# Optimization experiments

Hardware: AMD Instinct MI355X
Metric: run time of the kernel (lower is better)

Reference implementation:

```python
import jax, jax.numpy as jnp
import numpy as np

D_MODEL = 16   # output feature dim of channel_proj
D_STATE = 8
D_CONV = 2
D_INNER = 4    # expand * inner mamba d_model (2*2)
DT_RANK = 1    # ceil(2/16)
NUM_PAIRS = 36
B, W, T = 8, 8, 1024


def setup_inputs() -> dict:
    key = jax.random.key(0)
    ks = jax.random.split(key, 12)
    s = 0.5
    return {
        "raw_signals": jax.random.normal(ks[0], (B, W, NUM_PAIRS, 2, T), jnp.float32),
        "in_proj_w": jax.random.normal(ks[1], (2 * D_INNER, 2), jnp.float32) * s,
        "conv_w": jax.random.normal(ks[2], (D_INNER, D_CONV), jnp.float32) * s,
        "conv_b": jax.random.normal(ks[3], (D_INNER,), jnp.float32) * 0.1,
        "x_proj_w": jax.random.normal(ks[4], (DT_RANK + 2 * D_STATE, D_INNER), jnp.float32) * s,
        "dt_proj_w": jax.random.normal(ks[5], (D_INNER, DT_RANK), jnp.float32) * s,
        "dt_proj_b": jax.random.normal(ks[6], (D_INNER,), jnp.float32) * 0.1,
        # S4D-real init: A_log = log(arange(1..d_state)) per inner channel
        "A_log": jnp.log(jnp.broadcast_to(jnp.arange(1, D_STATE + 1, dtype=jnp.float32), (D_INNER, D_STATE))),
        "D_skip": jnp.ones((D_INNER,), jnp.float32),
        "out_proj_w": jax.random.normal(ks[7], (2, D_INNER), jnp.float32) * s,
        "proj_w": jax.random.normal(ks[8], (D_MODEL, 2), jnp.float32) * s,
        "proj_b": jax.random.normal(ks[9], (D_MODEL,), jnp.float32) * 0.1,
    }


def _mamba_forward(x_in, in_proj_w, conv_w, conv_b, x_proj_w, dt_proj_w,
                   dt_proj_b, A_log, D_skip, out_proj_w):
    # x_in: (N, T, 2)
    N, Tlen, _ = x_in.shape
    xz = jnp.einsum('ntc,dc->ntd', x_in, in_proj_w)          # (N,T,2*d_inner)
    x, z = jnp.split(xz, 2, axis=-1)                          # (N,T,d_inner) each
    # causal depthwise conv1d, kernel size D_CONV
    xp = jnp.pad(x, ((0, 0), (D_CONV - 1, 0), (0, 0)))
    x = sum(xp[:, k:k + Tlen] * conv_w[:, k] for k in range(D_CONV)) + conv_b
    x = jax.nn.silu(x)
    # input-dependent dt, B, C
    x_dbl = jnp.einsum('ntd,ed->nte', x, x_proj_w)            # (N,T,dt_rank+2*d_state)
    dt, Bm, Cm = jnp.split(x_dbl, [DT_RANK, DT_RANK + D_STATE], axis=-1)
    dt = jax.nn.softplus(jnp.einsum('ntr,dr->ntd', dt, dt_proj_w) + dt_proj_b)
    A = -jnp.exp(A_log)                                       # (d_inner,d_state)
    deltaA = jnp.exp(dt[..., None] * A)                       # (N,T,d_inner,d_state)
    deltaBx = dt[..., None] * Bm[:, :, None, :] * x[..., None]

    def step(h, inputs):
        dA_t, dBx_t, c_t = inputs
        h = dA_t * h + dBx_t                                  # (N,d_inner,d_state)
        y_t = jnp.einsum('nds,ns->nd', h, c_t)
        return h, y_t

    h0 = jnp.zeros((N, D_INNER, D_STATE), x.dtype)
    _, ys = jax.lax.scan(
        step, h0,
        (deltaA.transpose(1, 0, 2, 3), deltaBx.transpose(1, 0, 2, 3), Cm.transpose(1, 0, 2)))
    y = ys.transpose(1, 0, 2) + x * D_skip                    # (N,T,d_inner)
    y = y * jax.nn.silu(z)
    return jnp.einsum('ntd,cd->ntc', y, out_proj_w)           # (N,T,2)


def reference(raw_signals, in_proj_w, conv_w, conv_b, x_proj_w, dt_proj_w,
              dt_proj_b, A_log, D_skip, out_proj_w, proj_w, proj_b):
    Bsz, Wn, P, C, Tlen = raw_signals.shape
    # per-window loop in torch does identical math -> flatten windows into batch
    x_in = raw_signals.transpose(0, 1, 2, 4, 3).reshape(-1, Tlen, C)  # (B*W*P, T, 2)
    out = _mamba_forward(x_in, in_proj_w, conv_w, conv_b, x_proj_w, dt_proj_w,
                         dt_proj_b, A_log, D_skip, out_proj_w)
    feat = out.mean(axis=1)                                   # (B*W*P, 2)
    proj = jax.nn.relu(feat @ proj_w.T + proj_b)              # dropout is eval no-op
    proj = proj.reshape(Bsz, Wn, P, -1)                       # (B,W,P,d_model)
    return proj.mean(axis=2)                                  # (B,W,d_model)
```

## Files before the change

### kernel.cpp

```cpp
#include <hip/hip_runtime.h>
#include <hip/hip_fp16.h>


typedef float v2f __attribute__((ext_vector_type(2)));

#define TT 1024
#define TC 32
#define NSEGS 8
#define SEGLEN (TT / NSEGS)
#define NCHUNK (SEGLEN / TC)
#define NUM_PAIRS 36
#define NSEQ 2304

#define DTDS_ROW 34
#define BC_OFF 272
#define BC_STRIDE 36
#define PER_HALF_STRIDE 560
#define PER_WAVE (2 * PER_HALF_STRIDE)
#define STAGE_TOTAL (4 * PER_WAVE)

__device__ __forceinline__ float fast_silu(float v) {
    float e = __builtin_amdgcn_exp2f(v * -1.4426950408889634f);
    return v * __builtin_amdgcn_rcpf(1.0f + e);
}
__device__ __forceinline__ float fast_softplus(float v) {
    float e = __builtin_amdgcn_exp2f(v * 1.4426950408889634f);
    return __builtin_amdgcn_logf(1.0f + e) * 0.6931471805599453f;
}
__device__ __forceinline__ uint pk_h2(float a, float b) {
    return __builtin_bit_cast(uint, __builtin_amdgcn_cvt_pkrtz(a, b));
}

__global__ __launch_bounds__(256, 4)
void pm_kernel(const float* __restrict__ raw,
               const float* __restrict__ in_proj_w,
               const float* __restrict__ conv_w,
               const float* __restrict__ conv_b,
               const float* __restrict__ x_proj_w,
               const float* __restrict__ dt_proj_w,
               const float* __restrict__ dt_proj_b,
               const float* __restrict__ A_log,
               const float* __restrict__ D_skip,
               const float* __restrict__ out_proj_w,
               const float* __restrict__ proj_w,
               const float* __restrict__ proj_b,
               float* __restrict__ out)
{
    __shared__ float lds[STAGE_TOTAL];

    const int tid  = threadIdx.x;
    const int wid  = tid >> 6;
    const int lane = tid & 63;
    const int half = lane >> 5;
    const int lh   = lane & 31;
    const int g    = wid * 2 + half;
    const int n    = blockIdx.x;
    const float* rp = raw + (size_t)n * (2 * TT);

    float* hb = lds + wid * PER_WAVE + half * PER_HALF_STRIDE;

    v2f ipxy0[4], ipxy1[4];
#pragma unroll
    for (int d = 0; d < 4; ++d) {
        ipxy0[d] = (v2f){in_proj_w[2*d],     in_proj_w[2*(4+d)]};
        ipxy1[d] = (v2f){in_proj_w[2*d + 1], in_proj_w[2*(4+d) + 1]};
    }
    float cw0[4], cw1[4], cbv[4], dpw[4], dpb[4], Dsk[4], ow0[4], ow1[4], xp0[4];
#pragma unroll
    for (int d = 0; d < 4; ++d) {
        cw0[d] = conv_w[2*d]; cw1[d] = conv_w[2*d+1]; cbv[d] = conv_b[d];
        dpw[d] = dt_proj_w[d]; dpb[d] = dt_proj_b[d];
        Dsk[d] = D_skip[d]; ow0[d] = out_proj_w[d]; ow1[d] = out_proj_w[4+d];
        xp0[d] = x_proj_w[d];
    }
    v2f xbc[8][4];
#pragma unroll
    for (int s = 0; s < 8; ++s)
#pragma unroll
        for (int d = 0; d < 4; ++d)
            xbc[s][d] = (v2f){x_proj_w[4*(1+s) + d], x_proj_w[4*(9+s) + d]};

    const float LOG2E = 1.4426950408889634f;
    const int   d_idx = lh >> 3;
    const int   s_idx = lh & 7;
    const float A2ds  = -__expf(A_log[lh]) * LOG2E;
    const float owd0  = out_proj_w[d_idx];
    const float owd1  = out_proj_w[4 + d_idx];

    const float4* dp4 = (const float4*)hb + d_idx * (DTDS_ROW / 2);
    const uint4*  bp4 = (const uint4*)(hb + BC_OFF) + s_idx * (BC_STRIDE / 4);

    float A_run = 1.0f, hB = 0.0f, W = 0.0f, S = 0.0f;
    float sacc0 = 0.f, sacc1 = 0.f;
    float zf = 0.0f;

    const int seg0 = g * SEGLEN;

    int t0 = seg0 + lh;
    float c0  = rp[t0];
    float c1  = rp[TT + t0];
    float c0m = (t0 > 0) ? rp[t0 - 1]      : 0.0f;
    float c1m = (t0 > 0) ? rp[TT + t0 - 1] : 0.0f;

    for (int chunk = 0; chunk < NCHUNK; ++chunk) {
        float p0 = 0.f, p1 = 0.f, p0m = 0.f, p1m = 0.f;
        if (chunk + 1 < NCHUNK) {
            int tn = seg0 + (chunk + 1) * TC + lh;
            p0  = rp[tn];       p1  = rp[TT + tn];
            p0m = rp[tn - 1];   p1m = rp[TT + tn - 1];
        }

        float x[4], sz[4];
        v2f cc0 = (v2f){c0, c0}, cc1 = (v2f){c1, c1};
#pragma unroll
        for (int d = 0; d < 4; ++d) {
            v2f xv = __builtin_elementwise_fma(ipxy1[d], cc1, ipxy0[d] * cc0);
            float xm1 = ipxy0[d].x*c0m + ipxy1[d].x*c1m;
            float v   = xm1*cw0[d] + xv.x*cw1[d] + cbv[d];
            x[d]  = fast_silu(v);
            sz[d] = fast_silu(xv.y);
        }

        float dtin = xp0[0]*x[0] + xp0[1]*x[1] + xp0[2]*x[2] + xp0[3]*x[3];

        v2f bc[8];
#pragma unroll
        for (int s = 0; s < 8; ++s) {
            v2f a = xbc[s][0] * (v2f){x[0], x[0]};
            a = __builtin_elementwise_fma(xbc[s][1], (v2f){x[1], x[1]}, a);
            a = __builtin_elementwise_fma(xbc[s][2], (v2f){x[2], x[2]}, a);
            bc[s] = __builtin_elementwise_fma(xbc[s][3], (v2f){x[3], x[3]}, a);
        }

        float dt[4];
#pragma unroll
        for (int d = 0; d < 4; ++d) {
            dt[d] = fast_softplus(dtin*dpw[d] + dpb[d]);
            float g2 = x[d] * Dsk[d] * sz[d];
            sacc0 = fmaf(g2, ow0[d], sacc0);
            sacc1 = fmaf(g2, ow1[d], sacc1);
        }

        float2* dw = (float2*)hb;
#pragma unroll
        for (int d = 0; d < 4; ++d)
            dw[d*DTDS_ROW + lh] = make_float2(
                dt[d], __builtin_bit_cast(float, pk_h2(dt[d]*x[d], sz[d])));
        uint* bcw = (uint*)(hb + BC_OFF) + lh;
#pragma unroll
        for (int s = 0; s < 8; ++s)
            bcw[s * BC_STRIDE] = pk_h2(bc[s].x, bc[s].y);

#define SCAN_STEP(DTV, DSW, BCW) do {                                        \
            uint _ud = __builtin_bit_cast(uint, (DSW));                      \
            uint _ub = (BCW);                                                \
            float _b, _q;                                                    \
            asm("v_fma_mix_f32 %0, %1, %2, %3 op_sel_hi:[1,1,0]"             \
                : "=v"(_b) : "v"(_ud), "v"(_ub), "v"(zf));                   \
            asm("v_fma_mix_f32 %0, %1, %2, %3 op_sel:[1,1,0] op_sel_hi:[1,1,0]" \
                : "=v"(_q) : "v"(_ud), "v"(_ub), "v"(zf));                   \
            float _a = __builtin_amdgcn_exp2f((DTV) * A2ds);                 \
            A_run *= _a;                    \
            hB = fmaf(_a, hB, _b);          \
            W  = fmaf(A_run, _q, W);        \
            S  = fmaf(hB, _q, S);           \
        } while (0)

#pragma unroll
        for (int j = 0; j < TC / 4; ++j) {
            uint4  bq = bp4[j];
            float4 f0 = dp4[2*j];
            float4 f1 = dp4[2*j + 1];
            SCAN_STEP(f0.x, f0.y, bq.x);
            SCAN_STEP(f0.z, f0.w, bq.y);
            SCAN_STEP(f1.x, f1.y, bq.z);
            SCAN_STEP(f1.z, f1.w, bq.w);
        }
#undef SCAN_STEP

        c0 = p0; c1 = p1; c0m = p0m; c1m = p1m;
    }

    __syncthreads();
    float2* comb = (float2*)lds;
    comb[g*32 + lh] = make_float2(A_run, hB);
    __syncthreads();

    float h_in = 0.0f;
#pragma unroll
    for (int gg = 0; gg < NSEGS - 1; ++gg) {
        if (gg < g) {
            float2 abg = comb[gg*32 + lh];
            h_in = fmaf(abg.x, h_in, abg.y);
        }
    }

    float F = fmaf(h_in, W, S);
    float tot0 = fmaf(F, owd0, sacc0);
    float tot1 = fmaf(F, owd1, sacc1);
#pragma unroll
    for (int m = 16; m >= 1; m >>= 1) {
        tot0 += __shfl_xor(tot0, m, 64);
        tot1 += __shfl_xor(tot1, m, 64);
    }
    float* part = lds + 512;
    if (lh == 0) {
        part[g*2]     = tot0;
        part[g*2 + 1] = tot1;
    }
    __syncthreads();

    if (tid < 16) {
        float f0 = 0.f, f1 = 0.f;
#pragma unroll
        for (int gg = 0; gg < NSEGS; ++gg) {
            f0 += part[gg*2];
            f1 += part[gg*2 + 1];
        }
        f0 *= (1.0f / (float)TT);
        f1 *= (1.0f / (float)TT);
        float pv = f0*proj_w[2*tid] + f1*proj_w[2*tid + 1] + proj_b[tid];
        pv = fmaxf(pv, 0.0f);
        atomicAdd(out + (n / NUM_PAIRS) * 16 + tid, pv * (1.0f / NUM_PAIRS));
    }
}

extern "C" void kernel_launch(void* const* d_in, const int* in_sizes, int n_in,
                              void* d_out, int out_size, void* d_ws, size_t ws_size,
                              hipStream_t stream)
{
    const float* raw        = (const float*)d_in[0];
    const float* in_proj_w  = (const float*)d_in[1];
    const float* conv_w     = (const float*)d_in[2];
    const float* conv_b     = (const float*)d_in[3];
    const float* x_proj_w   = (const float*)d_in[4];
    const float* dt_proj_w  = (const float*)d_in[5];
    const float* dt_proj_b  = (const float*)d_in[6];
    const float* A_log      = (const float*)d_in[7];
    const float* D_skip     = (const float*)d_in[8];
    const float* out_proj_w = (const float*)d_in[9];
    const float* proj_w     = (const float*)d_in[10];
    const float* proj_b     = (const float*)d_in[11];

    hipMemsetAsync(d_out, 0, (size_t)out_size * sizeof(float), stream);

    pm_kernel<<<dim3(NSEQ), dim3(256), 0, stream>>>(
        raw, in_proj_w, conv_w, conv_b, x_proj_w, dt_proj_w, dt_proj_b,
        A_log, D_skip, out_proj_w, proj_w, proj_b, (float*)d_out);
}
```

Measured before the change: 117.0 us.

## Double-buffer LDS staging and software-pipeline pointwise stage ahead of scan

Replaces the per-chunk loop with a fully unrolled schedule that uses two LDS buffers per half-wave, so the pointwise work for the next chunk is issued before the scan of the current chunk. This lets independent math interleave with the serial scan dependency chain. It also separates the dt and packed dt*x/sz arrays into their own rows so each scan step loads one float4 per array, and it premultiplies dt by A with packed v2f multiplies. The cost is roughly double the LDS footprint and more live registers, which may lower occupancy.

```diff
diff --git a/kernel.cpp b/kernel.cpp
--- a/kernel.cpp
+++ b/kernel.cpp
@@ -12,12 +12,12 @@
 #define NUM_PAIRS 36
 #define NSEQ 2304
 
-#define DTDS_ROW 34
-#define BC_OFF 272
-#define BC_STRIDE 36
-#define PER_HALF_STRIDE 560
-#define PER_WAVE (2 * PER_HALF_STRIDE)
-#define STAGE_TOTAL (4 * PER_WAVE)
+#define ROWS 36
+#define DS_OFF 144
+#define BC_OFF 288
+#define PHS 592
+#define UNIT_STRIDE 1200
+#define STAGE_TOTAL (8 * UNIT_STRIDE)
 
 __device__ __forceinline__ float fast_silu(float v) {
     float e = __builtin_amdgcn_exp2f(v * -1.4426950408889634f);
@@ -57,7 +57,8 @@
     const int n    = blockIdx.x;
     const float* rp = raw + (size_t)n * (2 * TT);
 
-    float* hb = lds + wid * PER_WAVE + half * PER_HALF_STRIDE;
+    float* bufA = lds + g * UNIT_STRIDE;
+    float* bufB = bufA + PHS;
 
     v2f ipxy0[4], ipxy1[4];
 #pragma unroll
@@ -84,11 +85,9 @@
     const int   d_idx = lh >> 3;
     const int   s_idx = lh & 7;
     const float A2ds  = -__expf(A_log[lh]) * LOG2E;
+    const v2f   a2    = (v2f){A2ds, A2ds};
     const float owd0  = out_proj_w[d_idx];
     const float owd1  = out_proj_w[4 + d_idx];
-
-    const float4* dp4 = (const float4*)hb + d_idx * (DTDS_ROW / 2);
-    const uint4*  bp4 = (const uint4*)(hb + BC_OFF) + s_idx * (BC_STRIDE / 4);
 
     float A_run = 1.0f, hB = 0.0f, W = 0.0f, S = 0.0f;
     float sacc0 = 0.f, sacc1 = 0.f;
@@ -96,20 +95,7 @@
 
     const int seg0 = g * SEGLEN;
 
-    int t0 = seg0 + lh;
-    float c0  = rp[t0];
-    float c1  = rp[TT + t0];
-    float c0m = (t0 > 0) ? rp[t0 - 1]      : 0.0f;
-    float c1m = (t0 > 0) ? rp[TT + t0 - 1] : 0.0f;
-
-    for (int chunk = 0; chunk < NCHUNK; ++chunk) {
-        float p0 = 0.f, p1 = 0.f, p0m = 0.f, p1m = 0.f;
-        if (chunk + 1 < NCHUNK) {
-            int tn = seg0 + (chunk + 1) * TC + lh;
-            p0  = rp[tn];       p1  = rp[TT + tn];
-            p0m = rp[tn - 1];   p1m = rp[TT + tn - 1];
-        }
-
+    auto pw = [&](float c0, float c1, float c0m, float c1m, float* buf) {
         float x[4], sz[4];
         v2f cc0 = (v2f){c0, c0}, cc1 = (v2f){c1, c1};
 #pragma unroll
@@ -141,45 +127,78 @@
             sacc1 = fmaf(g2, ow1[d], sacc1);
         }
 
-        float2* dw = (float2*)hb;
-#pragma unroll
-        for (int d = 0; d < 4; ++d)
-            dw[d*DTDS_ROW + lh] = make_float2(
-                dt[d], __builtin_bit_cast(float, pk_h2(dt[d]*x[d], sz[d])));
-        uint* bcw = (uint*)(hb + BC_OFF) + lh;
+        uint* dsw = (uint*)(buf + DS_OFF) + lh;
+#pragma unroll
+        for (int d = 0; d < 4; ++d) {
+            buf[d*ROWS + lh] = dt[d];
+            dsw[d*ROWS] = pk_h2(dt[d]*x[d], sz[d]);
+        }
+        uint* bcw = (uint*)(buf + BC_OFF) + lh;
 #pragma unroll
         for (int s = 0; s < 8; ++s)
-            bcw[s * BC_STRIDE] = pk_h2(bc[s].x, bc[s].y);
-
-#define SCAN_STEP(DTV, DSW, BCW) do {                                        \
-            uint _ud = __builtin_bit_cast(uint, (DSW));                      \
+            bcw[s * ROWS] = pk_h2(bc[s].x, bc[s].y);
+    };
+
+#define SCAN_STEP(TA, DSW, BCW) do {                                         \
+            uint _ud = (DSW);                                                \
             uint _ub = (BCW);                                                \
             float _b, _q;                                                    \
             asm("v_fma_mix_f32 %0, %1, %2, %3 op_sel_hi:[1,1,0]"             \
                 : "=v"(_b) : "v"(_ud), "v"(_ub), "v"(zf));                   \
             asm("v_fma_mix_f32 %0, %1, %2, %3 op_sel:[1,1,0] op_sel_hi:[1,1,0]" \
                 : "=v"(_q) : "v"(_ud), "v"(_ub), "v"(zf));                   \
-            float _a = __builtin_amdgcn_exp2f((DTV) * A2ds);                 \
+            float _a = __builtin_amdgcn_exp2f(TA);                           \
             A_run *= _a;                    \
             hB = fmaf(_a, hB, _b);          \
             W  = fmaf(A_run, _q, W);        \
             S  = fmaf(hB, _q, S);           \
         } while (0)
 
+    auto scan = [&](const float* buf) {
+        const float4* dp4 = (const float4*)buf + d_idx * (ROWS/4);
+        const uint4*  sp4 = (const uint4*)(buf + DS_OFF) + d_idx * (ROWS/4);
+        const uint4*  bp4 = (const uint4*)(buf + BC_OFF) + s_idx * (ROWS/4);
 #pragma unroll
         for (int j = 0; j < TC / 4; ++j) {
+            float4 ft = dp4[j];
+            uint4  ds = sp4[j];
             uint4  bq = bp4[j];
-            float4 f0 = dp4[2*j];
-            float4 f1 = dp4[2*j + 1];
-            SCAN_STEP(f0.x, f0.y, bq.x);
-            SCAN_STEP(f0.z, f0.w, bq.y);
-            SCAN_STEP(f1.x, f1.y, bq.z);
-            SCAN_STEP(f1.z, f1.w, bq.w);
-        }
+            v2f t01 = (v2f){ft.x, ft.y} * a2;
+            v2f t23 = (v2f){ft.z, ft.w} * a2;
+            SCAN_STEP(t01.x, ds.x, bq.x);
+            SCAN_STEP(t01.y, ds.y, bq.y);
+            SCAN_STEP(t23.x, ds.z, bq.z);
+            SCAN_STEP(t23.y, ds.w, bq.w);
+        }
+    };
 #undef SCAN_STEP
 
-        c0 = p0; c1 = p1; c0m = p0m; c1m = p1m;
-    }
+    float r0, r1, r0m, r1m;
+    float s0, s1, s0m, s1m;
+    float u0, u1, u0m, u1m;
+    {
+        int t0 = seg0 + lh;
+        r0  = rp[t0];
+        r1  = rp[TT + t0];
+        r0m = (t0 > 0) ? rp[t0 - 1]      : 0.0f;
+        r1m = (t0 > 0) ? rp[TT + t0 - 1] : 0.0f;
+    }
+    {   int tn = seg0 + 1*TC + lh;
+        s0 = rp[tn]; s1 = rp[TT + tn]; s0m = rp[tn - 1]; s1m = rp[TT + tn - 1]; }
+
+    pw(r0, r1, r0m, r1m, bufA);
+    {   int tn = seg0 + 2*TC + lh;
+        u0 = rp[tn]; u1 = rp[TT + tn]; u0m = rp[tn - 1]; u1m = rp[TT + tn - 1]; }
+    pw(s0, s1, s0m, s1m, bufB);
+    {   int tn = seg0 + 3*TC + lh;
+        s0 = rp[tn]; s1 = rp[TT + tn]; s0m = rp[tn - 1]; s1m = rp[TT + tn - 1]; }
+
+    scan(bufA);
+    pw(u0, u1, u0m, u1m, bufA);
+    scan(bufB);
+    pw(s0, s1, s0m, s1m, bufB);
+    scan(bufA);
+    scan(bufB);
 
     __syncthreads();
     float2* comb = (float2*)lds;
```

Measured after the change: 254.3 us. +117.4%, slower.

## Halve segments per sequence and split dt/ds staging into separate LDS arrays

Applied to the files above, without the earlier changes.

Cuts the number of time segments per sequence from 8 to 4, so each block runs 128 threads (2 waves) and every lane scans twice as many chunks. The staging layout is reorganised: dt values and packed (dt*x, silu z) halves now sit in separate 36-wide rows, and each scan group reads one float4 of dt plus one uint4 of ds instead of two float4 of interleaved pairs. dt*A is computed with packed v2f multiplies. The aim is less cross-segment combine work and per-block overhead, at the price of a longer serial scan per lane and fewer waves per block.

```diff
diff --git a/kernel.cpp b/kernel.cpp
--- a/kernel.cpp
+++ b/kernel.cpp
@@ -6,18 +6,17 @@
 
 #define TT 1024
 #define TC 32
-#define NSEGS 8
+#define NSEGS 4
 #define SEGLEN (TT / NSEGS)
 #define NCHUNK (SEGLEN / TC)
 #define NUM_PAIRS 36
 #define NSEQ 2304
 
-#define DTDS_ROW 34
-#define BC_OFF 272
-#define BC_STRIDE 36
-#define PER_HALF_STRIDE 560
-#define PER_WAVE (2 * PER_HALF_STRIDE)
-#define STAGE_TOTAL (4 * PER_WAVE)
+#define ROWS 36
+#define DS_OFF 144
+#define BC_OFF 288
+#define UNIT_STRIDE 592
+#define STAGE_TOTAL (4 * UNIT_STRIDE)
 
 __device__ __forceinline__ float fast_silu(float v) {
     float e = __builtin_amdgcn_exp2f(v * -1.4426950408889634f);
@@ -31,7 +30,7 @@
     return __builtin_bit_cast(uint, __builtin_amdgcn_cvt_pkrtz(a, b));
 }
 
-__global__ __launch_bounds__(256, 4)
+__global__ __launch_bounds__(128, 4)
 void pm_kernel(const float* __restrict__ raw,
                const float* __restrict__ in_proj_w,
                const float* __restrict__ conv_w,
@@ -57,7 +56,7 @@
     const int n    = blockIdx.x;
     const float* rp = raw + (size_t)n * (2 * TT);
 
-    float* hb = lds + wid * PER_WAVE + half * PER_HALF_STRIDE;
+    float* hb = lds + g * UNIT_STRIDE;
 
     v2f ipxy0[4], ipxy1[4];
 #pragma unroll
@@ -84,11 +83,13 @@
     const int   d_idx = lh >> 3;
     const int   s_idx = lh & 7;
     const float A2ds  = -__expf(A_log[lh]) * LOG2E;
+    const v2f   a2    = (v2f){A2ds, A2ds};
     const float owd0  = out_proj_w[d_idx];
     const float owd1  = out_proj_w[4 + d_idx];
 
-    const float4* dp4 = (const float4*)hb + d_idx * (DTDS_ROW / 2);
-    const uint4*  bp4 = (const uint4*)(hb + BC_OFF) + s_idx * (BC_STRIDE / 4);
+    const float4* dp4 = (const float4*)hb + d_idx * (ROWS / 4);
+    const uint4*  sp4 = (const uint4*)(hb + DS_OFF) + d_idx * (ROWS / 4);
+    const uint4*  bp4 = (const uint4*)(hb + BC_OFF) + s_idx * (ROWS / 4);
 
     float A_run = 1.0f, hB = 0.0f, W = 0.0f, S = 0.0f;
     float sacc0 = 0.f, sacc1 = 0.f;
@@ -141,25 +142,26 @@
             sacc1 = fmaf(g2, ow1[d], sacc1);
         }
 
-        float2* dw = (float2*)hb;
-#pragma unroll
-        for (int d = 0; d < 4; ++d)
-            dw[d*DTDS_ROW + lh] = make_float2(
-                dt[d], __builtin_bit_cast(float, pk_h2(dt[d]*x[d], sz[d])));
+        uint* dsw = (uint*)(hb + DS_OFF) + lh;
+#pragma unroll
+        for (int d = 0; d < 4; ++d) {
+            hb[d*ROWS + lh] = dt[d];
+            dsw[d*ROWS] = pk_h2(dt[d]*x[d], sz[d]);
+        }
         uint* bcw = (uint*)(hb + BC_OFF) + lh;
 #pragma unroll
         for (int s = 0; s < 8; ++s)
-            bcw[s * BC_STRIDE] = pk_h2(bc[s].x, bc[s].y);
-
-#define SCAN_STEP(DTV, DSW, BCW) do {                                        \
-            uint _ud = __builtin_bit_cast(uint, (DSW));                      \
+            bcw[s * ROWS] = pk_h2(bc[s].x, bc[s].y);
+
+#define SCAN_STEP(TA, DSW, BCW) do {                                         \
+            uint _ud = (DSW);                                                \
             uint _ub = (BCW);                                                \
             float _b, _q;                                                    \
             asm("v_fma_mix_f32 %0, %1, %2, %3 op_sel_hi:[1,1,0]"             \
                 : "=v"(_b) : "v"(_ud), "v"(_ub), "v"(zf));                   \
             asm("v_fma_mix_f32 %0, %1, %2, %3 op_sel:[1,1,0] op_sel_hi:[1,1,0]" \
                 : "=v"(_q) : "v"(_ud), "v"(_ub), "v"(zf));                   \
-            float _a = __builtin_amdgcn_exp2f((DTV) * A2ds);                 \
+            float _a = __builtin_amdgcn_exp2f(TA);                           \
             A_run *= _a;                    \
             hB = fmaf(_a, hB, _b);          \
             W  = fmaf(A_run, _q, W);        \
@@ -168,13 +170,15 @@
 
 #pragma unroll
         for (int j = 0; j < TC / 4; ++j) {
+            float4 ft = dp4[j];
+            uint4  ds = sp4[j];
             uint4  bq = bp4[j];
-            float4 f0 = dp4[2*j];
-            float4 f1 = dp4[2*j + 1];
-            SCAN_STEP(f0.x, f0.y, bq.x);
-            SCAN_STEP(f0.z, f0.w, bq.y);
-            SCAN_STEP(f1.x, f1.y, bq.z);
-            SCAN_STEP(f1.z, f1.w, bq.w);
+            v2f t01 = (v2f){ft.x, ft.y} * a2;
+            v2f t23 = (v2f){ft.z, ft.w} * a2;
+            SCAN_STEP(t01.x, ds.x, bq.x);
+            SCAN_STEP(t01.y, ds.y, bq.y);
+            SCAN_STEP(t23.x, ds.z, bq.z);
+            SCAN_STEP(t23.y, ds.w, bq.w);
         }
 #undef SCAN_STEP
 
@@ -203,7 +207,7 @@
         tot0 += __shfl_xor(tot0, m, 64);
         tot1 += __shfl_xor(tot1, m, 64);
     }
-    float* part = lds + 512;
+    float* part = lds + 256;
     if (lh == 0) {
         part[g*2]     = tot0;
         part[g*2 + 1] = tot1;
@@ -244,7 +248,7 @@
 
     hipMemsetAsync(d_out, 0, (size_t)out_size * sizeof(float), stream);
 
-    pm_kernel<<<dim3(NSEQ), dim3(256), 0, stream>>>(
+    pm_kernel<<<dim3(NSEQ), dim3(128), 0, stream>>>(
         raw, in_proj_w, conv_w, conv_b, x_proj_w, dt_proj_w, dt_proj_b,
         A_log, D_skip, out_proj_w, proj_w, proj_b, (float*)d_out);
 }
```

After: 124.6 us. +6.5%, slower.
